# Performance work log

Hardware: AMD Instinct MI355X
Metric: run time of the kernel (lower is better)

## Reference

```python
import jax, jax.numpy as jnp
import numpy as np

N_NODES = 100000
N_EDGES = 1600000
IN_CH = 128
HID = 128
EPS = 1e-5


def setup_inputs() -> dict:
    key = jax.random.key(0)
    ks = jax.random.split(key, 16)
    x = jax.random.normal(ks[0], (N_NODES, IN_CH), dtype=jnp.float32)
    edge_index = jax.random.randint(ks[1], (2, N_EDGES), 0, N_NODES, dtype=jnp.int64)
    dims = [(IN_CH, HID), (HID, HID), (HID, HID // 2)]
    params = {}
    for i, (di, do) in enumerate(dims):
        params[f'w{i}'] = jax.random.normal(ks[2 + i], (di, do), dtype=jnp.float32) * (1.0 / np.sqrt(di))
        params[f'b{i}'] = jnp.zeros((do,), dtype=jnp.float32)
        params[f'g{i}'] = jnp.ones((do,), dtype=jnp.float32)
        params[f'be{i}'] = jnp.zeros((do,), dtype=jnp.float32)
    params['wc1'] = jax.random.normal(ks[8], (HID // 2, 32), dtype=jnp.float32) * (1.0 / np.sqrt(HID // 2))
    params['bc1'] = jnp.zeros((32,), dtype=jnp.float32)
    params['wc2'] = jax.random.normal(ks[9], (32, 1), dtype=jnp.float32) * (1.0 / np.sqrt(32))
    params['bc2'] = jnp.zeros((1,), dtype=jnp.float32)
    return {'x': x, 'edge_index': edge_index, **params}


def _gcn_forward(x, edge_index, w0, b0, g0, be0, w1, b1, g1, be1, w2, b2, g2, be2, wc1, bc1, wc2, bc2):
    n = x.shape[0]
    # add self-loops (GCNConv default)
    loops = jnp.arange(n, dtype=edge_index.dtype)
    src = jnp.concatenate([edge_index[0], loops])  # [E+N]
    dst = jnp.concatenate([edge_index[1], loops])
    # symmetric normalization: deg over targets (incl. self loops)
    deg = jax.ops.segment_sum(jnp.ones_like(dst, dtype=x.dtype), dst, num_segments=n)
    dis = jax.lax.rsqrt(jnp.maximum(deg, 1e-12))  # deg>=1 due to self loops
    norm = (dis[src] * dis[dst])[:, None]  # [E+N, 1]

    def layer(h, w, b, g, be):
        h = h @ w                                   # [N, d_out]
        h = jax.ops.segment_sum(h[src] * norm, dst, num_segments=n) + b
        mu = jnp.mean(h, axis=0)
        var = jnp.mean(jnp.square(h - mu), axis=0)  # biased var (torch BN)
        h = (h - mu) * jax.lax.rsqrt(var + EPS) * g + be
        return jax.nn.relu(h)                       # dropout: identity (eval)

    h = layer(x, w0, b0, g0, be0)
    h = layer(h, w1, b1, g1, be1)
    h = layer(h, w2, b2, g2, be2)
    h = jax.nn.relu(h @ wc1 + bc1)
    return (h @ wc2 + bc2)[:, 0]  # [N]


def reference(x, edge_index, w0, b0, g0, be0, w1, b1, g1, be1, w2, b2, g2, be2, wc1, bc1, wc2, bc2):
    return _gcn_forward(x, edge_index, w0, b0, g0, be0, w1, b1, g1, be1, w2, b2, g2, be2, wc1, bc1, wc2, bc2)
```

## Files before the change

kernel.cpp:

```cpp
#include <hip/hip_runtime.h>


typedef __attribute__((ext_vector_type(8))) short short8;
typedef __attribute__((ext_vector_type(4))) float f32x4;

#define BIN_SHIFT 7
#define BIN_NODES 128
#define CAPB 4096
#define CAP 64
#define SPARTS 1024
#define P1B 256

__device__ __forceinline__ float b2f(unsigned short u) {
    return __uint_as_float(((unsigned)u) << 16);
}
__device__ __forceinline__ unsigned short f2bf(float f) {
    unsigned u = __float_as_uint(f);
    return (unsigned short)((u + 0x7fff + ((u >> 16) & 1)) >> 16);
}

__global__ __launch_bounds__(256) void count_kernel(
    const int* __restrict__ eidx, int E, int nbins, int chunk,
    int* __restrict__ cntG,
    const float* __restrict__ w0, const float* __restrict__ w1,
    const float* __restrict__ w2, unsigned short* __restrict__ wf) {
    __shared__ int cntS[1024];
    int tid = threadIdx.x;
    for (int b = tid; b < 1024; b += 256) cntS[b] = 0;

    int tg = blockIdx.x * 256 + tid;
    if (tg < 40960) {
        const float* w;
        int idx, C;
        if (tg < 16384) { w = w0; idx = tg; C = 128; }
        else if (tg < 32768) { w = w1; idx = tg - 16384; C = 128; }
        else { w = w2; idx = tg - 32768; C = 64; }
        int j = idx & 7;
        int lane = (idx >> 3) & 63;
        int q = (idx >> 9) & 3;
        int n_tile = idx >> 11;
        int k = q * 32 + (lane >> 4) * 8 + j;
        int n = n_tile * 16 + (lane & 15);
        wf[tg] = f2bf(w[k * C + n]);
    }
    __syncthreads();
    int e0 = blockIdx.x * chunk;
    int e1 = min(e0 + chunk, E);
    for (int e = e0 + tid; e < e1; e += 256)
        atomicAdd(&cntS[eidx[E + e] >> BIN_SHIFT], 1);
    __syncthreads();
    for (int b = tid; b < nbins; b += 256)
        cntG[b * P1B + blockIdx.x] = cntS[b];
}

__global__ __launch_bounds__(P1B) void scan_kernel(int* __restrict__ cntG,
                                                   int* __restrict__ bin_fill) {
    __shared__ int sh[P1B];
    int b = blockIdx.x, t = threadIdx.x;
    int v = cntG[b * P1B + t];
    sh[t] = v;
    __syncthreads();
    for (int d = 1; d < P1B; d <<= 1) {
        int u = (t >= d) ? sh[t - d] : 0;
        __syncthreads();
        sh[t] += u;
        __syncthreads();
    }
    cntG[b * P1B + t] = sh[t] - v;
    if (t == P1B - 1) bin_fill[b] = sh[P1B - 1];
}

__global__ __launch_bounds__(256) void place_kernel(
    const int* __restrict__ eidx, int E, int nbins, int chunk,
    const int* __restrict__ baseG, int* __restrict__ binned) {
    __shared__ int cntS[1024];
    __shared__ int baseS[1024];
    int tid = threadIdx.x;
    for (int b = tid; b < nbins; b += 256) {
        baseS[b] = baseG[b * P1B + blockIdx.x];
        cntS[b] = 0;
    }
    __syncthreads();
    int e0 = blockIdx.x * chunk;
    int e1 = min(e0 + chunk, E);
    for (int e = e0 + tid; e < e1; e += 256) {
        int d = eidx[E + e];
        int s = eidx[e];
        int b = d >> BIN_SHIFT;
        int p = baseS[b] + atomicAdd(&cntS[b], 1);
        if (p < CAPB) binned[b * CAPB + p] = (s << BIN_SHIFT) | (d & (BIN_NODES - 1));
    }
}

__global__ __launch_bounds__(256) void part2_kernel(const int* __restrict__ bin_fill,
                                                    const int* __restrict__ binned,
                                                    int N, int* __restrict__ fill,
                                                    float* __restrict__ dis,
                                                    int* __restrict__ stage) {
    __shared__ int lfill[BIN_NODES];
    int b = blockIdx.x, tid = threadIdx.x;
    if (tid < BIN_NODES) lfill[tid] = 0;
    __syncthreads();
    int cnt = min(bin_fill[b], CAPB);
    const int* seg = binned + b * CAPB;
    for (int i = tid; i < cnt; i += 256) {
        int v = seg[i];
        int dl = v & (BIN_NODES - 1);
        int p = atomicAdd(&lfill[dl], 1);
        int node = (b << BIN_SHIFT) + dl;
        if (p < CAP) stage[(node << 6) + p] = v >> BIN_SHIFT;
    }
    __syncthreads();
    if (tid < BIN_NODES) {
        int node = (b << BIN_SHIFT) + tid;
        if (node < N) {
            int c = lfill[tid];
            fill[node] = c;
            dis[node] = rsqrtf((float)c + 1.0f);
        }
    }
}

__device__ __forceinline__ void load8(const float* p, float4& lo, float4& hi) {
    lo = *(const float4*)p;
    hi = *(const float4*)(p + 4);
}
__device__ __forceinline__ void load8(const unsigned short* p, float4& lo, float4& hi) {
    int4 q = *(const int4*)p;
    lo = make_float4(__uint_as_float((unsigned)q.x << 16),
                     __uint_as_float((unsigned)q.x & 0xffff0000u),
                     __uint_as_float((unsigned)q.y << 16),
                     __uint_as_float((unsigned)q.y & 0xffff0000u));
    hi = make_float4(__uint_as_float((unsigned)q.z << 16),
                     __uint_as_float((unsigned)q.z & 0xffff0000u),
                     __uint_as_float((unsigned)q.w << 16),
                     __uint_as_float((unsigned)q.w & 0xffff0000u));
}

template <int C, typename InT>
__global__ __launch_bounds__(256, 5) void mfma_gemm_kernel(
    const InT* __restrict__ xin, const unsigned short* __restrict__ wf,
    const float* __restrict__ scale, const float* __restrict__ shift,
    const float* __restrict__ dis, unsigned short* __restrict__ out, int N) {
    constexpr int NT = C / 16;
    constexpr int WFRAGS = NT * 4 * 64;
    __shared__ short8 ws[WFRAGS];
    int tid = threadIdx.x;
    for (int i = tid; i < WFRAGS; i += 256) ws[i] = ((const short8*)wf)[i];

    int lane = tid & 63;
    int wave = tid >> 6;
    int m0 = blockIdx.x * 64 + wave * 16;
    int r15 = lane & 15, r4 = lane >> 4;
    f32x4 acc[NT];
#pragma unroll
    for (int t = 0; t < NT; t++) acc[t] = (f32x4){0.f, 0.f, 0.f, 0.f};
    int row0 = m0 + r15;
    int row0c = min(row0, N - 1);
    __syncthreads();

#pragma unroll
    for (int q = 0; q < 4; q++) {
        int kb = q * 32 + r4 * 8;
        float4 a0l, a0h;
        load8(xin + (size_t)row0c * 128 + kb, a0l, a0h);
        if (scale) {
            float4 scl = *(const float4*)&scale[kb];
            float4 sch = *(const float4*)&scale[kb + 4];
            float4 shl = *(const float4*)&shift[kb];
            float4 shh = *(const float4*)&shift[kb + 4];
            a0l.x = fmaxf(a0l.x * scl.x + shl.x, 0.f);
            a0l.y = fmaxf(a0l.y * scl.y + shl.y, 0.f);
            a0l.z = fmaxf(a0l.z * scl.z + shl.z, 0.f);
            a0l.w = fmaxf(a0l.w * scl.w + shl.w, 0.f);
            a0h.x = fmaxf(a0h.x * sch.x + shh.x, 0.f);
            a0h.y = fmaxf(a0h.y * sch.y + shh.y, 0.f);
            a0h.z = fmaxf(a0h.z * sch.z + shh.z, 0.f);
            a0h.w = fmaxf(a0h.w * sch.w + shh.w, 0.f);
        }
        short8 a0;
        a0[0] = (short)f2bf(a0l.x); a0[1] = (short)f2bf(a0l.y);
        a0[2] = (short)f2bf(a0l.z); a0[3] = (short)f2bf(a0l.w);
        a0[4] = (short)f2bf(a0h.x); a0[5] = (short)f2bf(a0h.y);
        a0[6] = (short)f2bf(a0h.z); a0[7] = (short)f2bf(a0h.w);
#pragma unroll
        for (int nt = 0; nt < NT; nt++) {
            short8 b = ws[(nt * 4 + q) * 64 + lane];
            acc[nt] = __builtin_amdgcn_mfma_f32_16x16x32_bf16(a0, b, acc[nt], 0, 0, 0);
        }
    }
    float d0r[4];
#pragma unroll
    for (int r = 0; r < 4; r++) {
        int rowa = m0 + r4 * 4 + r;
        d0r[r] = (rowa < N) ? dis[rowa] : 0.f;
    }
#pragma unroll
    for (int nt = 0; nt < NT; nt++) {
        int col = nt * 16 + r15;
#pragma unroll
        for (int r = 0; r < 4; r++) {
            int rowa = m0 + r4 * 4 + r;
            if (rowa < N) out[(size_t)rowa * C + col] = f2bf(acc[nt][r] * d0r[r]);
        }
    }
}

__global__ __launch_bounds__(256) void agg128_kernel(
    const unsigned short* __restrict__ h, const int* __restrict__ fill,
    const int* __restrict__ stage, const float* __restrict__ dis,
    unsigned short* __restrict__ out, int N) {
    int lane = threadIdx.x & 63;
    int node = blockIdx.x * 4 + (threadIdx.x >> 6);
    if (node >= N) return;
    float dn = dis[node];
    ushort2 sv = ((const ushort2*)(h + (size_t)node * 128))[lane];
    float2 acc = make_float2(b2f(sv.x), b2f(sv.y));
    int ne = min(fill[node], CAP);
    int pk = (lane < ne) ? stage[(node << 6) + lane] : 0;
    int j = 0;
    for (; j + 16 <= ne; j += 16) {
        ushort2 a[16];
#pragma unroll
        for (int t = 0; t < 16; t++) {
            int s = __builtin_amdgcn_readlane(pk, j + t);
            a[t] = ((const ushort2*)(h + (size_t)s * 128))[lane];
        }
#pragma unroll
        for (int t = 0; t < 16; t++) { acc.x += b2f(a[t].x); acc.y += b2f(a[t].y); }
    }
    for (; j + 8 <= ne; j += 8) {
        ushort2 a[8];
#pragma unroll
        for (int t = 0; t < 8; t++) {
            int s = __builtin_amdgcn_readlane(pk, j + t);
            a[t] = ((const ushort2*)(h + (size_t)s * 128))[lane];
        }
#pragma unroll
        for (int t = 0; t < 8; t++) { acc.x += b2f(a[t].x); acc.y += b2f(a[t].y); }
    }
    for (; j + 4 <= ne; j += 4) {
        ushort2 a[4];
#pragma unroll
        for (int t = 0; t < 4; t++) {
            int s = __builtin_amdgcn_readlane(pk, j + t);
            a[t] = ((const ushort2*)(h + (size_t)s * 128))[lane];
        }
#pragma unroll
        for (int t = 0; t < 4; t++) { acc.x += b2f(a[t].x); acc.y += b2f(a[t].y); }
    }
    for (; j < ne; j++) {
        int s = __builtin_amdgcn_readlane(pk, j);
        ushort2 a = ((const ushort2*)(h + (size_t)s * 128))[lane];
        acc.x += b2f(a.x);
        acc.y += b2f(a.y);
    }
    ((ushort2*)(out + (size_t)node * 128))[lane] =
        make_ushort2(f2bf(acc.x * dn), f2bf(acc.y * dn));
}

__global__ __launch_bounds__(256) void agg64_kernel(
    const unsigned short* __restrict__ h, const int* __restrict__ fill,
    const int* __restrict__ stage, const float* __restrict__ dis,
    unsigned short* __restrict__ out, int N) {
    int lane = threadIdx.x & 63;
    int node = blockIdx.x * 4 + (threadIdx.x >> 6);
    if (node >= N) return;
    int half = lane >> 5, ch = lane & 31;
    float dn = dis[node];
    float2 acc = make_float2(0.f, 0.f);
    if (half == 0) {
        ushort2 sv = ((const ushort2*)(h + (size_t)node * 64))[ch];
        acc.x = b2f(sv.x);
        acc.y = b2f(sv.y);
    }
    int ne = min(fill[node], CAP);
    int pk = (lane < ne) ? stage[(node << 6) + lane] : 0;
    int j = 0;
    for (; j + 16 <= ne; j += 16) {
        ushort2 a[8];
#pragma unroll
        for (int t = 0; t < 8; t++) {
            int s = __shfl(pk, j + 2 * t + half);
            a[t] = ((const ushort2*)(h + (size_t)s * 64))[ch];
        }
#pragma unroll
        for (int t = 0; t < 8; t++) { acc.x += b2f(a[t].x); acc.y += b2f(a[t].y); }
    }
    for (; j + 8 <= ne; j += 8) {
        ushort2 a[4];
#pragma unroll
        for (int t = 0; t < 4; t++) {
            int s = __shfl(pk, j + 2 * t + half);
            a[t] = ((const ushort2*)(h + (size_t)s * 64))[ch];
        }
#pragma unroll
        for (int t = 0; t < 4; t++) { acc.x += b2f(a[t].x); acc.y += b2f(a[t].y); }
    }
    for (; j < ne; j += 2) {
        int jj = j + half;
        int s = __shfl(pk, jj);
        bool v = jj < ne;
        ushort2 a = ((const ushort2*)(h + (size_t)s * 64))[ch];
        acc.x += v ? b2f(a.x) : 0.f;
        acc.y += v ? b2f(a.y) : 0.f;
    }
    acc.x += __shfl_down(acc.x, 32);
    acc.y += __shfl_down(acc.y, 32);
    if (half == 0)
        ((ushort2*)(out + (size_t)node * 64))[ch] =
            make_ushort2(f2bf(acc.x * dn), f2bf(acc.y * dn));
}

template <int C>
__global__ __launch_bounds__(256) void stats1_kernel(const unsigned short* __restrict__ h,
                                                     int N, float* __restrict__ partials) {
    constexpr int CG = C / 4;
    constexpr int RG = 256 / CG;
    int t = threadIdx.x;
    int cg = t % CG;
    int rg = t / CG;
    float s[4] = {0.f, 0.f, 0.f, 0.f}, q[4] = {0.f, 0.f, 0.f, 0.f};
    for (int n = blockIdx.x * RG + rg; n < N; n += gridDim.x * RG) {
        ushort4 v = *(const ushort4*)&h[(size_t)n * C + cg * 4];
        float f0 = b2f(v.x), f1 = b2f(v.y), f2 = b2f(v.z), f3 = b2f(v.w);
        s[0] += f0; s[1] += f1; s[2] += f2; s[3] += f3;
        q[0] += f0 * f0; q[1] += f1 * f1; q[2] += f2 * f2; q[3] += f3 * f3;
    }
    __shared__ float red[256 * 8];
#pragma unroll
    for (int k = 0; k < 4; k++) {
        red[(rg * CG + cg) * 8 + k] = s[k];
        red[(rg * CG + cg) * 8 + 4 + k] = q[k];
    }
    __syncthreads();
    if (rg == 0) {
#pragma unroll
        for (int w = 1; w < RG; w++)
#pragma unroll
            for (int k = 0; k < 4; k++) {
                s[k] += red[(w * CG + cg) * 8 + k];
                q[k] += red[(w * CG + cg) * 8 + 4 + k];
            }
        float* pb = partials + (size_t)blockIdx.x * 2 * C;
#pragma unroll
        for (int k = 0; k < 4; k++) {
            pb[cg * 4 + k] = s[k];
            pb[C + cg * 4 + k] = q[k];
        }
    }
}

template <int C>
__global__ __launch_bounds__(256) void stats2_kernel(const float* __restrict__ partials,
                                                     const float* __restrict__ g,
                                                     const float* __restrict__ be, int N,
                                                     float* __restrict__ scale,
                                                     float* __restrict__ shift) {
    int c = blockIdx.x;
    int t = threadIdx.x;
    float s = 0.f, q = 0.f;
    for (int b = t; b < SPARTS; b += 256) {
        const float* pb = partials + (size_t)b * 2 * C;
        s += pb[c];
        q += pb[C + c];
    }
    __shared__ float rs[256], rq[256];
    rs[t] = s;
    rq[t] = q;
    __syncthreads();
    for (int d = 128; d > 0; d >>= 1) {
        if (t < d) {
            rs[t] += rs[t + d];
            rq[t] += rq[t + d];
        }
        __syncthreads();
    }
    if (t == 0) {
        float inv_n = 1.0f / (float)N;
        float mean = rs[0] * inv_n;
        float var = rq[0] * inv_n - mean * mean;
        var = var > 0.f ? var : 0.f;
        float sc = g[c] * rsqrtf(var + 1e-5f);
        scale[c] = sc;
        shift[c] = be[c] - mean * sc;
    }
}

__global__ __launch_bounds__(256) void head_kernel(
    const unsigned short* __restrict__ h, const float* __restrict__ scale,
    const float* __restrict__ shift, const float* __restrict__ wc1,
    const float* __restrict__ bc1, const float* __restrict__ wc2,
    const float* __restrict__ bc2, float* __restrict__ out, int N) {
    __shared__ float w1s[64 * 32];
    __shared__ float b1s[32], w2s[32], s2s[64], sh2[64];
    __shared__ float b2s;
    int tid = threadIdx.x;
    for (int i = tid; i < 64 * 32; i += 256) w1s[i] = wc1[i];
    if (tid < 32) { b1s[tid] = bc1[tid]; w2s[tid] = wc2[tid]; }
    if (tid < 64) { s2s[tid] = scale[tid]; sh2[tid] = shift[tid]; }
    if (tid == 0) b2s = bc2[0];
    __syncthreads();
    int n = blockIdx.x * 256 + tid;
    if (n >= N) return;
    float v[64];
#pragma unroll
    for (int k = 0; k < 64; k++) {
        float x = b2f(h[(size_t)n * 64 + k]) * s2s[k] + sh2[k];
        v[k] = x > 0.f ? x : 0.f;
    }
    float o = b2s;
#pragma unroll 2
    for (int j = 0; j < 32; j++) {
        float t = b1s[j];
#pragma unroll
        for (int k = 0; k < 64; k++) t += v[k] * w1s[k * 32 + j];
        t = t > 0.f ? t : 0.f;
        o += t * w2s[j];
    }
    out[n] = o;
}

extern "C" void kernel_launch(void* const* d_in, const int* in_sizes, int n_in,
                              void* d_out, int out_size, void* d_ws, size_t ws_size,
                              hipStream_t stream) {
    const float* x = (const float*)d_in[0];
    const int* eidx = (const int*)d_in[1];
    const float* w0 = (const float*)d_in[2];
    const float* g0 = (const float*)d_in[4];
    const float* be0 = (const float*)d_in[5];
    const float* w1 = (const float*)d_in[6];
    const float* g1 = (const float*)d_in[8];
    const float* be1 = (const float*)d_in[9];
    const float* w2 = (const float*)d_in[10];
    const float* g2 = (const float*)d_in[12];
    const float* be2 = (const float*)d_in[13];
    const float* wc1 = (const float*)d_in[14];
    const float* bc1 = (const float*)d_in[15];
    const float* wc2 = (const float*)d_in[16];
    const float* bc2 = (const float*)d_in[17];

    const int N = in_sizes[0] / 128;
    const int E = in_sizes[1] / 2;
    const int nbins = (N + BIN_NODES - 1) >> BIN_SHIFT;

    char* p = (char*)d_ws;
    auto alloc = [&](size_t bytes) {
        void* r = (void*)p;
        p += (bytes + 255) & ~(size_t)255;
        return r;
    };
    int* bin_fill = (int*)alloc((size_t)nbins * 4);
    int* fill = (int*)alloc((size_t)N * 4);
    int* binned = (int*)alloc((size_t)nbins * CAPB * 4);
    int* stage = (int*)alloc((size_t)N * CAP * 4);
    float* dis = (float*)alloc((size_t)N * 4);
    float* ss = (float*)alloc(3 * 256 * 4);
    float* partials = (float*)alloc((size_t)SPARTS * 256 * 4);
    unsigned short* hA = (unsigned short*)alloc((size_t)N * 128 * 2);
    unsigned short* hB = (unsigned short*)alloc((size_t)N * 128 * 2);
    unsigned short* wf = (unsigned short*)alloc(40960 * 2);
    unsigned short* wf0 = wf;
    unsigned short* wf1 = wf + 16384;
    unsigned short* wf2 = wf + 32768;

    float* sc0 = ss, *sh0 = ss + 128;
    float* sc1 = ss + 256, *sh1 = ss + 384;
    float* sc2 = ss + 512, *sh2 = ss + 640;

    int* cntG = (int*)partials;

    int chunk = (E + P1B - 1) / P1B;
    count_kernel<<<P1B, 256, 0, stream>>>(eidx, E, nbins, chunk, cntG, w0, w1, w2, wf);
    scan_kernel<<<nbins, P1B, 0, stream>>>(cntG, bin_fill);
    place_kernel<<<P1B, 256, 0, stream>>>(eidx, E, nbins, chunk, cntG, binned);
    part2_kernel<<<nbins, 256, 0, stream>>>(bin_fill, binned, N, fill, dis, stage);

    int agg_grid = (N + 3) / 4;
    int gemm_grid = (N + 63) / 64;

    mfma_gemm_kernel<128, float><<<gemm_grid, 256, 0, stream>>>(x, wf0, nullptr, nullptr,
                                                                dis, hA, N);
    agg128_kernel<<<agg_grid, 256, 0, stream>>>(hA, fill, stage, dis, hB, N);
    stats1_kernel<128><<<SPARTS, 256, 0, stream>>>(hB, N, partials);
    stats2_kernel<128><<<128, 256, 0, stream>>>(partials, g0, be0, N, sc0, sh0);

    mfma_gemm_kernel<128, unsigned short><<<gemm_grid, 256, 0, stream>>>(
        hB, wf1, sc0, sh0, dis, hA, N);
    agg128_kernel<<<agg_grid, 256, 0, stream>>>(hA, fill, stage, dis, hB, N);
    stats1_kernel<128><<<SPARTS, 256, 0, stream>>>(hB, N, partials);
    stats2_kernel<128><<<128, 256, 0, stream>>>(partials, g1, be1, N, sc1, sh1);

    mfma_gemm_kernel<64, unsigned short><<<gemm_grid, 256, 0, stream>>>(
        hB, wf2, sc1, sh1, dis, hA, N);
    agg64_kernel<<<agg_grid, 256, 0, stream>>>(hA, fill, stage, dis, hB, N);
    stats1_kernel<64><<<SPARTS, 256, 0, stream>>>(hB, N, partials);
    stats2_kernel<64><<<64, 256, 0, stream>>>(partials, g2, be2, N, sc2, sh2);

    head_kernel<<<(N + 255) / 256, 256, 0, stream>>>(hB, sc2, sh2, wc1, bc1, wc2,
                                                     bc2, (float*)d_out, N);
}
```

Before: 436.2 us.

## Fuse preprocessing, stats, and GEMM kernels into cooperative persistent kernels with grid sync

Replaces separate launches for edge binning, weight conversion, GEMM, BN statistics, and head with three cooperative kernels that use grid-wide barriers between phases. The launch count and inter-kernel gaps are cut, and grid size is chosen from occupancy queries. In exchange, each phase now runs in a persistent grid with grid syncs. The count phase uses fewer blocks if occupancy is low, and the fused kernels may carry more shared memory and registers.

```diff
diff --git a/kernel.cpp b/kernel.cpp
--- a/kernel.cpp
+++ b/kernel.cpp
@@ -1,4 +1,7 @@
 #include <hip/hip_runtime.h>
+#include <hip/hip_cooperative_groups.h>
+
+namespace cg = cooperative_groups;
 
 
 typedef __attribute__((ext_vector_type(8))) short short8;
@@ -8,8 +11,6 @@
 #define BIN_NODES 128
 #define CAPB 4096
 #define CAP 64
-#define SPARTS 1024
-#define P1B 256
 
 __device__ __forceinline__ float b2f(unsigned short u) {
     return __uint_as_float(((unsigned)u) << 16);
@@ -17,108 +18,6 @@
 __device__ __forceinline__ unsigned short f2bf(float f) {
     unsigned u = __float_as_uint(f);
     return (unsigned short)((u + 0x7fff + ((u >> 16) & 1)) >> 16);
-}
-
-__global__ __launch_bounds__(256) void count_kernel(
-    const int* __restrict__ eidx, int E, int nbins, int chunk,
-    int* __restrict__ cntG,
-    const float* __restrict__ w0, const float* __restrict__ w1,
-    const float* __restrict__ w2, unsigned short* __restrict__ wf) {
-    __shared__ int cntS[1024];
-    int tid = threadIdx.x;
-    for (int b = tid; b < 1024; b += 256) cntS[b] = 0;
-
-    int tg = blockIdx.x * 256 + tid;
-    if (tg < 40960) {
-        const float* w;
-        int idx, C;
-        if (tg < 16384) { w = w0; idx = tg; C = 128; }
-        else if (tg < 32768) { w = w1; idx = tg - 16384; C = 128; }
-        else { w = w2; idx = tg - 32768; C = 64; }
-        int j = idx & 7;
-        int lane = (idx >> 3) & 63;
-        int q = (idx >> 9) & 3;
-        int n_tile = idx >> 11;
-        int k = q * 32 + (lane >> 4) * 8 + j;
-        int n = n_tile * 16 + (lane & 15);
-        wf[tg] = f2bf(w[k * C + n]);
-    }
-    __syncthreads();
-    int e0 = blockIdx.x * chunk;
-    int e1 = min(e0 + chunk, E);
-    for (int e = e0 + tid; e < e1; e += 256)
-        atomicAdd(&cntS[eidx[E + e] >> BIN_SHIFT], 1);
-    __syncthreads();
-    for (int b = tid; b < nbins; b += 256)
-        cntG[b * P1B + blockIdx.x] = cntS[b];
-}
-
-__global__ __launch_bounds__(P1B) void scan_kernel(int* __restrict__ cntG,
-                                                   int* __restrict__ bin_fill) {
-    __shared__ int sh[P1B];
-    int b = blockIdx.x, t = threadIdx.x;
-    int v = cntG[b * P1B + t];
-    sh[t] = v;
-    __syncthreads();
-    for (int d = 1; d < P1B; d <<= 1) {
-        int u = (t >= d) ? sh[t - d] : 0;
-        __syncthreads();
-        sh[t] += u;
-        __syncthreads();
-    }
-    cntG[b * P1B + t] = sh[t] - v;
-    if (t == P1B - 1) bin_fill[b] = sh[P1B - 1];
-}
-
-__global__ __launch_bounds__(256) void place_kernel(
-    const int* __restrict__ eidx, int E, int nbins, int chunk,
-    const int* __restrict__ baseG, int* __restrict__ binned) {
-    __shared__ int cntS[1024];
-    __shared__ int baseS[1024];
-    int tid = threadIdx.x;
-    for (int b = tid; b < nbins; b += 256) {
-        baseS[b] = baseG[b * P1B + blockIdx.x];
-        cntS[b] = 0;
-    }
-    __syncthreads();
-    int e0 = blockIdx.x * chunk;
-    int e1 = min(e0 + chunk, E);
-    for (int e = e0 + tid; e < e1; e += 256) {
-        int d = eidx[E + e];
-        int s = eidx[e];
-        int b = d >> BIN_SHIFT;
-        int p = baseS[b] + atomicAdd(&cntS[b], 1);
-        if (p < CAPB) binned[b * CAPB + p] = (s << BIN_SHIFT) | (d & (BIN_NODES - 1));
-    }
-}
-
-__global__ __launch_bounds__(256) void part2_kernel(const int* __restrict__ bin_fill,
-                                                    const int* __restrict__ binned,
-                                                    int N, int* __restrict__ fill,
-                                                    float* __restrict__ dis,
-                                                    int* __restrict__ stage) {
-    __shared__ int lfill[BIN_NODES];
-    int b = blockIdx.x, tid = threadIdx.x;
-    if (tid < BIN_NODES) lfill[tid] = 0;
-    __syncthreads();
-    int cnt = min(bin_fill[b], CAPB);
-    const int* seg = binned + b * CAPB;
-    for (int i = tid; i < cnt; i += 256) {
-        int v = seg[i];
-        int dl = v & (BIN_NODES - 1);
-        int p = atomicAdd(&lfill[dl], 1);
-        int node = (b << BIN_SHIFT) + dl;
-        if (p < CAP) stage[(node << 6) + p] = v >> BIN_SHIFT;
-    }
-    __syncthreads();
-    if (tid < BIN_NODES) {
-        int node = (b << BIN_SHIFT) + tid;
-        if (node < N) {
-            int c = lfill[tid];
-            fill[node] = c;
-            dis[node] = rsqrtf((float)c + 1.0f);
-        }
-    }
 }
 
 __device__ __forceinline__ void load8(const float* p, float4& lo, float4& hi) {
@@ -137,74 +36,352 @@
                      __uint_as_float((unsigned)q.w & 0xffff0000u));
 }
 
+
+__device__ void wfrag_phase(const float* __restrict__ w0, const float* __restrict__ w1,
+                            const float* __restrict__ w2, unsigned short* __restrict__ wf) {
+    int tg = blockIdx.x * 256 + threadIdx.x;
+    if (tg >= 40960) return;
+    const float* w;
+    int idx, C;
+    if (tg < 16384) { w = w0; idx = tg; C = 128; }
+    else if (tg < 32768) { w = w1; idx = tg - 16384; C = 128; }
+    else { w = w2; idx = tg - 32768; C = 64; }
+    int j = idx & 7;
+    int lane = (idx >> 3) & 63;
+    int q = (idx >> 9) & 3;
+    int n_tile = idx >> 11;
+    int k = q * 32 + (lane >> 4) * 8 + j;
+    int n = n_tile * 16 + (lane & 15);
+    wf[tg] = f2bf(w[k * C + n]);
+}
+
+__device__ void count_phase(const int* __restrict__ eidx, int E, int CB, int chunk,
+                            int nbins, int* __restrict__ cntG, int* cntS) {
+    int tid = threadIdx.x;
+    if (blockIdx.x >= CB) return;
+    for (int b = tid; b < 1024; b += 256) cntS[b] = 0;
+    __syncthreads();
+    int e0 = blockIdx.x * chunk;
+    int e1 = min(e0 + chunk, E);
+    for (int e = e0 + tid; e < e1; e += 256)
+        atomicAdd(&cntS[eidx[E + e] >> BIN_SHIFT], 1);
+    __syncthreads();
+    for (int b = tid; b < nbins; b += 256) cntG[b * CB + blockIdx.x] = cntS[b];
+}
+
+__device__ void scan_phase(int nbins, int CB, int* __restrict__ cntG,
+                           int* __restrict__ bin_fill, int* sh) {
+    int t = threadIdx.x;
+    for (int b = blockIdx.x; b < nbins; b += gridDim.x) {
+        int v = (t < CB) ? cntG[b * CB + t] : 0;
+        sh[t] = v;
+        __syncthreads();
+        for (int d = 1; d < 256; d <<= 1) {
+            int u = (t >= d) ? sh[t - d] : 0;
+            __syncthreads();
+            sh[t] += u;
+            __syncthreads();
+        }
+        if (t < CB) cntG[b * CB + t] = sh[t] - v;
+        if (t == 255) bin_fill[b] = sh[255];
+        __syncthreads();
+    }
+}
+
+__device__ void place_phase(const int* __restrict__ eidx, int E, int CB, int chunk,
+                            int nbins, const int* __restrict__ baseG,
+                            int* __restrict__ binned, int* cntS, int* baseS) {
+    int tid = threadIdx.x;
+    if (blockIdx.x >= CB) return;
+    for (int b = tid; b < nbins; b += 256) {
+        baseS[b] = baseG[b * CB + blockIdx.x];
+        cntS[b] = 0;
+    }
+    __syncthreads();
+    int e0 = blockIdx.x * chunk;
+    int e1 = min(e0 + chunk, E);
+    for (int e = e0 + tid; e < e1; e += 256) {
+        int d = eidx[E + e];
+        int s = eidx[e];
+        int b = d >> BIN_SHIFT;
+        int p = baseS[b] + atomicAdd(&cntS[b], 1);
+        if (p < CAPB) binned[b * CAPB + p] = (s << BIN_SHIFT) | (d & (BIN_NODES - 1));
+    }
+}
+
+__device__ void part2_phase(const int* __restrict__ bin_fill, const int* __restrict__ binned,
+                            int N, int* __restrict__ fill, float* __restrict__ dis,
+                            int* __restrict__ stg, int* lfill) {
+    int nb = (N + BIN_NODES - 1) >> BIN_SHIFT;
+    int tid = threadIdx.x;
+    for (int b = blockIdx.x; b < nb; b += gridDim.x) {
+        if (tid < BIN_NODES) lfill[tid] = 0;
+        __syncthreads();
+        int cnt = min(bin_fill[b], CAPB);
+        const int* seg = binned + b * CAPB;
+        for (int i = tid; i < cnt; i += 256) {
+            int v = seg[i];
+            int dl = v & (BIN_NODES - 1);
+            int pp = atomicAdd(&lfill[dl], 1);
+            int node = (b << BIN_SHIFT) + dl;
+            if (pp < CAP) stg[(node << 6) + pp] = v >> BIN_SHIFT;
+        }
+        __syncthreads();
+        if (tid < BIN_NODES) {
+            int node = (b << BIN_SHIFT) + tid;
+            if (node < N) {
+                int c = lfill[tid];
+                fill[node] = c;
+                dis[node] = rsqrtf((float)c + 1.0f);
+            }
+        }
+        __syncthreads();
+    }
+}
+
+template <int C>
+__device__ void stage_w_phase(const unsigned short* __restrict__ wfp, short8* ws) {
+    constexpr int WFRAGS = (C / 16) * 4 * 64;
+    for (int i = threadIdx.x; i < WFRAGS; i += 256) ws[i] = ((const short8*)wfp)[i];
+}
+
 template <int C, typename InT>
-__global__ __launch_bounds__(256, 5) void mfma_gemm_kernel(
-    const InT* __restrict__ xin, const unsigned short* __restrict__ wf,
-    const float* __restrict__ scale, const float* __restrict__ shift,
-    const float* __restrict__ dis, unsigned short* __restrict__ out, int N) {
+__device__ void gemm_tiles_phase(const InT* __restrict__ xin,
+                                 const float* __restrict__ scale,
+                                 const float* __restrict__ shift,
+                                 const float* __restrict__ dis,
+                                 unsigned short* __restrict__ out, int N,
+                                 const short8* ws) {
     constexpr int NT = C / 16;
-    constexpr int WFRAGS = NT * 4 * 64;
-    __shared__ short8 ws[WFRAGS];
     int tid = threadIdx.x;
-    for (int i = tid; i < WFRAGS; i += 256) ws[i] = ((const short8*)wf)[i];
-
     int lane = tid & 63;
     int wave = tid >> 6;
-    int m0 = blockIdx.x * 64 + wave * 16;
     int r15 = lane & 15, r4 = lane >> 4;
-    f32x4 acc[NT];
-#pragma unroll
-    for (int t = 0; t < NT; t++) acc[t] = (f32x4){0.f, 0.f, 0.f, 0.f};
-    int row0 = m0 + r15;
-    int row0c = min(row0, N - 1);
-    __syncthreads();
-
-#pragma unroll
-    for (int q = 0; q < 4; q++) {
-        int kb = q * 32 + r4 * 8;
-        float4 a0l, a0h;
-        load8(xin + (size_t)row0c * 128 + kb, a0l, a0h);
-        if (scale) {
-            float4 scl = *(const float4*)&scale[kb];
-            float4 sch = *(const float4*)&scale[kb + 4];
-            float4 shl = *(const float4*)&shift[kb];
-            float4 shh = *(const float4*)&shift[kb + 4];
-            a0l.x = fmaxf(a0l.x * scl.x + shl.x, 0.f);
-            a0l.y = fmaxf(a0l.y * scl.y + shl.y, 0.f);
-            a0l.z = fmaxf(a0l.z * scl.z + shl.z, 0.f);
-            a0l.w = fmaxf(a0l.w * scl.w + shl.w, 0.f);
-            a0h.x = fmaxf(a0h.x * sch.x + shh.x, 0.f);
-            a0h.y = fmaxf(a0h.y * sch.y + shh.y, 0.f);
-            a0h.z = fmaxf(a0h.z * sch.z + shh.z, 0.f);
-            a0h.w = fmaxf(a0h.w * sch.w + shh.w, 0.f);
-        }
-        short8 a0;
-        a0[0] = (short)f2bf(a0l.x); a0[1] = (short)f2bf(a0l.y);
-        a0[2] = (short)f2bf(a0l.z); a0[3] = (short)f2bf(a0l.w);
-        a0[4] = (short)f2bf(a0h.x); a0[5] = (short)f2bf(a0h.y);
-        a0[6] = (short)f2bf(a0h.z); a0[7] = (short)f2bf(a0h.w);
-#pragma unroll
-        for (int nt = 0; nt < NT; nt++) {
-            short8 b = ws[(nt * 4 + q) * 64 + lane];
-            acc[nt] = __builtin_amdgcn_mfma_f32_16x16x32_bf16(a0, b, acc[nt], 0, 0, 0);
-        }
-    }
-    float d0r[4];
-#pragma unroll
-    for (int r = 0; r < 4; r++) {
-        int rowa = m0 + r4 * 4 + r;
-        d0r[r] = (rowa < N) ? dis[rowa] : 0.f;
-    }
-#pragma unroll
-    for (int nt = 0; nt < NT; nt++) {
-        int col = nt * 16 + r15;
+    int ntiles = (N + 63) / 64;
+    for (int bx = blockIdx.x; bx < ntiles; bx += gridDim.x) {
+        int m0 = bx * 64 + wave * 16;
+        f32x4 acc[NT];
+#pragma unroll
+        for (int t = 0; t < NT; t++) acc[t] = (f32x4){0.f, 0.f, 0.f, 0.f};
+        int row0c = min(m0 + r15, N - 1);
+#pragma unroll
+        for (int q = 0; q < 4; q++) {
+            int kb = q * 32 + r4 * 8;
+            float4 a0l, a0h;
+            load8(xin + (size_t)row0c * 128 + kb, a0l, a0h);
+            if (scale) {
+                float4 scl = *(const float4*)&scale[kb];
+                float4 sch = *(const float4*)&scale[kb + 4];
+                float4 shl = *(const float4*)&shift[kb];
+                float4 shh = *(const float4*)&shift[kb + 4];
+                a0l.x = fmaxf(a0l.x * scl.x + shl.x, 0.f);
+                a0l.y = fmaxf(a0l.y * scl.y + shl.y, 0.f);
+                a0l.z = fmaxf(a0l.z * scl.z + shl.z, 0.f);
+                a0l.w = fmaxf(a0l.w * scl.w + shl.w, 0.f);
+                a0h.x = fmaxf(a0h.x * sch.x + shh.x, 0.f);
+                a0h.y = fmaxf(a0h.y * sch.y + shh.y, 0.f);
+                a0h.z = fmaxf(a0h.z * sch.z + shh.z, 0.f);
+                a0h.w = fmaxf(a0h.w * sch.w + shh.w, 0.f);
+            }
+            short8 a0;
+            a0[0] = (short)f2bf(a0l.x); a0[1] = (short)f2bf(a0l.y);
+            a0[2] = (short)f2bf(a0l.z); a0[3] = (short)f2bf(a0l.w);
+            a0[4] = (short)f2bf(a0h.x); a0[5] = (short)f2bf(a0h.y);
+            a0[6] = (short)f2bf(a0h.z); a0[7] = (short)f2bf(a0h.w);
+#pragma unroll
+            for (int nt = 0; nt < NT; nt++) {
+                short8 b = ws[(nt * 4 + q) * 64 + lane];
+                acc[nt] = __builtin_amdgcn_mfma_f32_16x16x32_bf16(a0, b, acc[nt], 0, 0, 0);
+            }
+        }
+        float d0r[4];
 #pragma unroll
         for (int r = 0; r < 4; r++) {
             int rowa = m0 + r4 * 4 + r;
-            if (rowa < N) out[(size_t)rowa * C + col] = f2bf(acc[nt][r] * d0r[r]);
-        }
-    }
-}
+            d0r[r] = (rowa < N) ? dis[rowa] : 0.f;
+        }
+#pragma unroll
+        for (int nt = 0; nt < NT; nt++) {
+            int col = nt * 16 + r15;
+#pragma unroll
+            for (int r = 0; r < 4; r++) {
+                int rowa = m0 + r4 * 4 + r;
+                if (rowa < N) out[(size_t)rowa * C + col] = f2bf(acc[nt][r] * d0r[r]);
+            }
+        }
+    }
+}
+
+template <int C>
+__device__ void stats1_phase(const unsigned short* __restrict__ h, int N,
+                             float* __restrict__ partials, float* red) {
+    constexpr int CG = C / 4;
+    constexpr int RG = 256 / CG;
+    int t = threadIdx.x;
+    int cgi = t % CG;
+    int rg = t / CG;
+    float s[4] = {0.f, 0.f, 0.f, 0.f}, q[4] = {0.f, 0.f, 0.f, 0.f};
+    for (int n = blockIdx.x * RG + rg; n < N; n += gridDim.x * RG) {
+        ushort4 v = *(const ushort4*)&h[(size_t)n * C + cgi * 4];
+        float f0 = b2f(v.x), f1 = b2f(v.y), f2 = b2f(v.z), f3 = b2f(v.w);
+        s[0] += f0; s[1] += f1; s[2] += f2; s[3] += f3;
+        q[0] += f0 * f0; q[1] += f1 * f1; q[2] += f2 * f2; q[3] += f3 * f3;
+    }
+#pragma unroll
+    for (int k = 0; k < 4; k++) {
+        red[(rg * CG + cgi) * 8 + k] = s[k];
+        red[(rg * CG + cgi) * 8 + 4 + k] = q[k];
+    }
+    __syncthreads();
+    if (rg == 0) {
+#pragma unroll
+        for (int w = 1; w < RG; w++)
+#pragma unroll
+            for (int k = 0; k < 4; k++) {
+                s[k] += red[(w * CG + cgi) * 8 + k];
+                q[k] += red[(w * CG + cgi) * 8 + 4 + k];
+            }
+        float* pb = partials + (size_t)blockIdx.x * 2 * C;
+#pragma unroll
+        for (int k = 0; k < 4; k++) {
+            pb[cgi * 4 + k] = s[k];
+            pb[C + cgi * 4 + k] = q[k];
+        }
+    }
+    __syncthreads();
+}
+
+template <int C>
+__device__ void stats2_phase(const float* __restrict__ partials, const float* __restrict__ g,
+                             const float* __restrict__ be, int N,
+                             float* __restrict__ scale, float* __restrict__ shift) {
+    __shared__ float rs[256], rq[256];
+    int t = threadIdx.x;
+    int nparts = gridDim.x;
+    for (int c = blockIdx.x; c < C; c += gridDim.x) {
+        float s = 0.f, q = 0.f;
+        for (int b = t; b < nparts; b += 256) {
+            const float* pb = partials + (size_t)b * 2 * C;
+            s += pb[c];
+            q += pb[C + c];
+        }
+        rs[t] = s;
+        rq[t] = q;
+        __syncthreads();
+        for (int d = 128; d > 0; d >>= 1) {
+            if (t < d) {
+                rs[t] += rs[t + d];
+                rq[t] += rq[t + d];
+            }
+            __syncthreads();
+        }
+        if (t == 0) {
+            float inv_n = 1.0f / (float)N;
+            float mean = rs[0] * inv_n;
+            float var = rq[0] * inv_n - mean * mean;
+            var = var > 0.f ? var : 0.f;
+            float sc = g[c] * rsqrtf(var + 1e-5f);
+            scale[c] = sc;
+            shift[c] = be[c] - mean * sc;
+        }
+        __syncthreads();
+    }
+}
+
+__device__ void head_stage(const float* __restrict__ wc1, const float* __restrict__ bc1,
+                           const float* __restrict__ wc2, const float* __restrict__ bc2,
+                           float* w1s, float* b1s, float* w2s, float* b2s) {
+    int tid = threadIdx.x;
+    for (int i = tid; i < 64 * 32; i += 256) w1s[i] = wc1[i];
+    if (tid < 32) { b1s[tid] = bc1[tid]; w2s[tid] = wc2[tid]; }
+    if (tid == 0) b2s[0] = bc2[0];
+}
+
+__device__ void head_compute(const unsigned short* __restrict__ h,
+                             const float* __restrict__ scale, const float* __restrict__ shift,
+                             float* __restrict__ out, int N, const float* w1s,
+                             const float* b1s, const float* w2s, const float* b2s,
+                             float* s2s, float* sh2v) {
+    int tid = threadIdx.x;
+    if (tid < 64) { s2s[tid] = scale[tid]; sh2v[tid] = shift[tid]; }
+    __syncthreads();
+    for (int bx = blockIdx.x; bx * 256 < N; bx += gridDim.x) {
+        int n = bx * 256 + tid;
+        if (n < N) {
+            float v[64];
+#pragma unroll
+            for (int k = 0; k < 64; k++) {
+                float xv = b2f(h[(size_t)n * 64 + k]) * s2s[k] + sh2v[k];
+                v[k] = xv > 0.f ? xv : 0.f;
+            }
+            float o = b2s[0];
+#pragma unroll 2
+            for (int j = 0; j < 32; j++) {
+                float t = b1s[j];
+#pragma unroll
+                for (int k = 0; k < 64; k++) t += v[k] * w1s[k * 32 + j];
+                t = t > 0.f ? t : 0.f;
+                o += t * w2s[j];
+            }
+            out[n] = o;
+        }
+    }
+}
+
+
+__global__ __launch_bounds__(256, 4) void fusedA_kernel(
+    const int* eidx, int E, int nbins, int CB, int chunk, int* cntG, int* bin_fill,
+    int* binned, int N, int* fill, float* dis, int* stg, const float* w0,
+    const float* w1, const float* w2, unsigned short* wf, const float* x,
+    unsigned short* hA) {
+    __shared__ __align__(16) int ibuf[8192];
+    __shared__ int lfill[BIN_NODES];
+    cg::grid_group grid = cg::this_grid();
+    wfrag_phase(w0, w1, w2, wf);
+    count_phase(eidx, E, CB, chunk, nbins, cntG, ibuf);
+    grid.sync();
+    scan_phase(nbins, CB, cntG, bin_fill, ibuf);
+    grid.sync();
+    place_phase(eidx, E, CB, chunk, nbins, cntG, binned, ibuf, ibuf + 1024);
+    grid.sync();
+    part2_phase(bin_fill, binned, N, fill, dis, stg, lfill);
+    stage_w_phase<128>(wf, (short8*)ibuf);
+    grid.sync();
+    gemm_tiles_phase<128, float>(x, (const float*)nullptr, (const float*)nullptr,
+                                 dis, hA, N, (const short8*)ibuf);
+}
+
+template <int CS, int CO>
+__global__ __launch_bounds__(256, 4) void fusedB_kernel(
+    const unsigned short* hin, const float* g, const float* be, float* partials,
+    float* scale, float* shift, const unsigned short* wfp, const float* dis,
+    unsigned short* hout, int N) {
+    __shared__ __align__(16) float fbuf[8192];
+    cg::grid_group grid = cg::this_grid();
+    stats1_phase<CS>(hin, N, partials, fbuf);
+    grid.sync();
+    stats2_phase<CS>(partials, g, be, N, scale, shift);
+    stage_w_phase<CO>(wfp, (short8*)fbuf);
+    grid.sync();
+    gemm_tiles_phase<CO, unsigned short>(hin, scale, shift, dis, hout, N,
+                                         (const short8*)fbuf);
+}
+
+__global__ __launch_bounds__(256, 4) void fusedC_kernel(
+    const unsigned short* hin, const float* g, const float* be, float* partials,
+    float* scale, float* shift, const float* wc1, const float* bc1, const float* wc2,
+    const float* bc2, float* out, int N) {
+    __shared__ __align__(16) float fbuf[2048];
+    __shared__ float b1s[32], w2s[32], s2s[64], sh2v[64], b2sv[1];
+    cg::grid_group grid = cg::this_grid();
+    stats1_phase<64>(hin, N, partials, fbuf);
+    grid.sync();
+    stats2_phase<64>(partials, g, be, N, scale, shift);
+    head_stage(wc1, bc1, wc2, bc2, fbuf, b1s, w2s, b2sv);
+    grid.sync();
+    head_compute(hin, scale, shift, out, N, fbuf, b1s, w2s, b2sv, s2s, sh2v);
+}
+
 
 __global__ __launch_bounds__(256) void agg128_kernel(
     const unsigned short* __restrict__ h, const int* __restrict__ fill,
@@ -312,114 +489,6 @@
             make_ushort2(f2bf(acc.x * dn), f2bf(acc.y * dn));
 }
 
-template <int C>
-__global__ __launch_bounds__(256) void stats1_kernel(const unsigned short* __restrict__ h,
-                                                     int N, float* __restrict__ partials) {
-    constexpr int CG = C / 4;
-    constexpr int RG = 256 / CG;
-    int t = threadIdx.x;
-    int cg = t % CG;
-    int rg = t / CG;
-    float s[4] = {0.f, 0.f, 0.f, 0.f}, q[4] = {0.f, 0.f, 0.f, 0.f};
-    for (int n = blockIdx.x * RG + rg; n < N; n += gridDim.x * RG) {
-        ushort4 v = *(const ushort4*)&h[(size_t)n * C + cg * 4];
-        float f0 = b2f(v.x), f1 = b2f(v.y), f2 = b2f(v.z), f3 = b2f(v.w);
-        s[0] += f0; s[1] += f1; s[2] += f2; s[3] += f3;
-        q[0] += f0 * f0; q[1] += f1 * f1; q[2] += f2 * f2; q[3] += f3 * f3;
-    }
-    __shared__ float red[256 * 8];
-#pragma unroll
-    for (int k = 0; k < 4; k++) {
-        red[(rg * CG + cg) * 8 + k] = s[k];
-        red[(rg * CG + cg) * 8 + 4 + k] = q[k];
-    }
-    __syncthreads();
-    if (rg == 0) {
-#pragma unroll
-        for (int w = 1; w < RG; w++)
-#pragma unroll
-            for (int k = 0; k < 4; k++) {
-                s[k] += red[(w * CG + cg) * 8 + k];
-                q[k] += red[(w * CG + cg) * 8 + 4 + k];
-            }
-        float* pb = partials + (size_t)blockIdx.x * 2 * C;
-#pragma unroll
-        for (int k = 0; k < 4; k++) {
-            pb[cg * 4 + k] = s[k];
-            pb[C + cg * 4 + k] = q[k];
-        }
-    }
-}
-
-template <int C>
-__global__ __launch_bounds__(256) void stats2_kernel(const float* __restrict__ partials,
-                                                     const float* __restrict__ g,
-                                                     const float* __restrict__ be, int N,
-                                                     float* __restrict__ scale,
-                                                     float* __restrict__ shift) {
-    int c = blockIdx.x;
-    int t = threadIdx.x;
-    float s = 0.f, q = 0.f;
-    for (int b = t; b < SPARTS; b += 256) {
-        const float* pb = partials + (size_t)b * 2 * C;
-        s += pb[c];
-        q += pb[C + c];
-    }
-    __shared__ float rs[256], rq[256];
-    rs[t] = s;
-    rq[t] = q;
-    __syncthreads();
-    for (int d = 128; d > 0; d >>= 1) {
-        if (t < d) {
-            rs[t] += rs[t + d];
-            rq[t] += rq[t + d];
-        }
-        __syncthreads();
-    }
-    if (t == 0) {
-        float inv_n = 1.0f / (float)N;
-        float mean = rs[0] * inv_n;
-        float var = rq[0] * inv_n - mean * mean;
-        var = var > 0.f ? var : 0.f;
-        float sc = g[c] * rsqrtf(var + 1e-5f);
-        scale[c] = sc;
-        shift[c] = be[c] - mean * sc;
-    }
-}
-
-__global__ __launch_bounds__(256) void head_kernel(
-    const unsigned short* __restrict__ h, const float* __restrict__ scale,
-    const float* __restrict__ shift, const float* __restrict__ wc1,
-    const float* __restrict__ bc1, const float* __restrict__ wc2,
-    const float* __restrict__ bc2, float* __restrict__ out, int N) {
-    __shared__ float w1s[64 * 32];
-    __shared__ float b1s[32], w2s[32], s2s[64], sh2[64];
-    __shared__ float b2s;
-    int tid = threadIdx.x;
-    for (int i = tid; i < 64 * 32; i += 256) w1s[i] = wc1[i];
-    if (tid < 32) { b1s[tid] = bc1[tid]; w2s[tid] = wc2[tid]; }
-    if (tid < 64) { s2s[tid] = scale[tid]; sh2[tid] = shift[tid]; }
-    if (tid == 0) b2s = bc2[0];
-    __syncthreads();
-    int n = blockIdx.x * 256 + tid;
-    if (n >= N) return;
-    float v[64];
-#pragma unroll
-    for (int k = 0; k < 64; k++) {
-        float x = b2f(h[(size_t)n * 64 + k]) * s2s[k] + sh2[k];
-        v[k] = x > 0.f ? x : 0.f;
-    }
-    float o = b2s;
-#pragma unroll 2
-    for (int j = 0; j < 32; j++) {
-        float t = b1s[j];
-#pragma unroll
-        for (int k = 0; k < 64; k++) t += v[k] * w1s[k * 32 + j];
-        t = t > 0.f ? t : 0.f;
-        o += t * w2s[j];
-    }
-    out[n] = o;
-}
 
 extern "C" void kernel_launch(void* const* d_in, const int* in_sizes, int n_in,
                               void* d_out, int out_size, void* d_ws, size_t ws_size,
@@ -439,6 +508,7 @@
     const float* bc1 = (const float*)d_in[15];
     const float* wc2 = (const float*)d_in[16];
     const float* bc2 = (const float*)d_in[17];
+    float* outp = (float*)d_out;
 
     const int N = in_sizes[0] / 128;
     const int E = in_sizes[1] / 2;
@@ -456,47 +526,60 @@
     int* stage = (int*)alloc((size_t)N * CAP * 4);
     float* dis = (float*)alloc((size_t)N * 4);
     float* ss = (float*)alloc(3 * 256 * 4);
-    float* partials = (float*)alloc((size_t)SPARTS * 256 * 4);
+    float* partials = (float*)alloc((size_t)1024 * 256 * 4);
     unsigned short* hA = (unsigned short*)alloc((size_t)N * 128 * 2);
     unsigned short* hB = (unsigned short*)alloc((size_t)N * 128 * 2);
     unsigned short* wf = (unsigned short*)alloc(40960 * 2);
-    unsigned short* wf0 = wf;
     unsigned short* wf1 = wf + 16384;
     unsigned short* wf2 = wf + 32768;
 
     float* sc0 = ss, *sh0 = ss + 128;
     float* sc1 = ss + 256, *sh1 = ss + 384;
     float* sc2 = ss + 512, *sh2 = ss + 640;
-
     int* cntG = (int*)partials;
 
-    int chunk = (E + P1B - 1) / P1B;
-    count_kernel<<<P1B, 256, 0, stream>>>(eidx, E, nbins, chunk, cntG, w0, w1, w2, wf);
-    scan_kernel<<<nbins, P1B, 0, stream>>>(cntG, bin_fill);
-    place_kernel<<<P1B, 256, 0, stream>>>(eidx, E, nbins, chunk, cntG, binned);
-    part2_kernel<<<nbins, 256, 0, stream>>>(bin_fill, binned, N, fill, dis, stage);
-
+    static int occA = 0, occB1 = 0, occB2 = 0, occC = 0;
+    if (occA == 0) {
+        hipOccupancyMaxActiveBlocksPerMultiprocessor(&occA, (const void*)fusedA_kernel, 256, 0);
+        hipOccupancyMaxActiveBlocksPerMultiprocessor(&occB1, (const void*)fusedB_kernel<128, 128>, 256, 0);
+        hipOccupancyMaxActiveBlocksPerMultiprocessor(&occB2, (const void*)fusedB_kernel<128, 64>, 256, 0);
+        hipOccupancyMaxActiveBlocksPerMultiprocessor(&occC, (const void*)fusedC_kernel, 256, 0);
+        if (occA < 1) occA = 1;
+        if (occB1 < 1) occB1 = 1;
+        if (occB2 < 1) occB2 = 1;
+        if (occC < 1) occC = 1;
+    }
+    auto clampg = [](int occ) {
+        int g = occ * 256;
+        return g > 1024 ? 1024 : g;
+    };
+    int gA = clampg(occA), gB1 = clampg(occB1), gB2 = clampg(occB2), gC = clampg(occC);
+
+    int CB = gA < 256 ? gA : 256;
+    int chunk = (E + CB - 1) / CB;
+    int Nv = N, Ev = E, nbv = nbins, CBv = CB, chv = chunk;
+
+    {
+        void* a[] = {(void*)&eidx, &Ev, &nbv, &CBv, &chv, &cntG, &bin_fill, &binned,
+                     &Nv, &fill, &dis, &stage, (void*)&w0, (void*)&w1, (void*)&w2,
+                     &wf, (void*)&x, &hA};
+        hipLaunchCooperativeKernel((const void*)fusedA_kernel, dim3(gA), dim3(256), a, 0, stream);
+    }
     int agg_grid = (N + 3) / 4;
-    int gemm_grid = (N + 63) / 64;
-
-    mfma_gemm_kernel<128, float><<<gemm_grid, 256, 0, stream>>>(x, wf0, nullptr, nullptr,
-                                                                dis, hA, N);
     agg128_kernel<<<agg_grid, 256, 0, stream>>>(hA, fill, stage, dis, hB, N);
-    stats1_kernel<128><<<SPARTS, 256, 0, stream>>>(hB, N, partials);
-    stats2_kernel<128><<<128, 256, 0, stream>>>(partials, g0, be0, N, sc0, sh0);
-
-    mfma_gemm_kernel<128, unsigned short><<<gemm_grid, 256, 0, stream>>>(
-        hB, wf1, sc0, sh0, dis, hA, N);
+    {
+        void* a[] = {&hB, (void*)&g0, (void*)&be0, &partials, &sc0, &sh0, &wf1, &dis, &hA, &Nv};
+        hipLaunchCooperativeKernel((const void*)fusedB_kernel<128, 128>, dim3(gB1), dim3(256), a, 0, stream);
+    }
     agg128_kernel<<<agg_grid, 256, 0, stream>>>(hA, fill, stage, dis, hB, N);
-    stats1_kernel<128><<<SPARTS, 256, 0, stream>>>(hB, N, partials);
-    stats2_kernel<128><<<128, 256, 0, stream>>>(partials, g1, be1, N, sc1, sh1);
-
-    mfma_gemm_kernel<64, unsigned short><<<gemm_grid, 256, 0, stream>>>(
-        hB, wf2, sc1, sh1, dis, hA, N);
+    {
+        void* a[] = {&hB, (void*)&g1, (void*)&be1, &partials, &sc1, &sh1, &wf2, &dis, &hA, &Nv};
+        hipLaunchCooperativeKernel((const void*)fusedB_kernel<128, 64>, dim3(gB2), dim3(256), a, 0, stream);
+    }
     agg64_kernel<<<agg_grid, 256, 0, stream>>>(hA, fill, stage, dis, hB, N);
-    stats1_kernel<64><<<SPARTS, 256, 0, stream>>>(hB, N, partials);
-    stats2_kernel<64><<<64, 256, 0, stream>>>(partials, g2, be2, N, sc2, sh2);
-
-    head_kernel<<<(N + 255) / 256, 256, 0, stream>>>(hB, sc2, sh2, wc1, bc1, wc2,
-                                                     bc2, (float*)d_out, N);
-}
+    {
+        void* a[] = {&hB, (void*)&g2, (void*)&be2, &partials, &sc2, &sh2,
+                     (void*)&wc1, (void*)&bc1, (void*)&wc2, (void*)&bc2, &outp, &Nv};
+        hipLaunchCooperativeKernel((const void*)fusedC_kernel, dim3(gC), dim3(256), a, 0, stream);
+    }
+}
```

Result: slower. 1.121 ms (+157.1%).
